# Performance work log

Hardware: AMD Instinct MI355X
Metric: run time of the kernel (lower is better)

The kernel has to match this reference:

```python
import jax, jax.numpy as jnp
import numpy as np

B, T, E, H = 8, 2048, 1024, 1024
_LN_EPS = 1e-3  # keras LayerNormalization default epsilon


def _ln(x, g, b):
    mu = jnp.mean(x, axis=-1, keepdims=True)
    var = jnp.var(x, axis=-1, keepdims=True)
    return (x - mu) * jax.lax.rsqrt(var + _LN_EPS) * g + b


def _time_shift(x):
    # ZeroPadding1D((1,0)) applied to x[:, :-1]: shift right by one, zero at t=0
    return jnp.pad(x[:, :-1], ((0, 0), (1, 0), (0, 0)))


def _wkv(k, v, w, u):
    """RWKV-v4 wkv: numerically stabilized exponential-decay recurrence.
    k, v: (B, T, H); w = -exp(time_decay) (negative), u = time_first: (H,).
    wkv_t = (sum_{i<t} e^{(t-1-i)w + k_i} v_i + e^{u + k_t} v_t)
          / (sum_{i<t} e^{(t-1-i)w + k_i}     + e^{u + k_t})
    """
    Bk, Tk, Hk = k.shape

    def step(carry, kv_t):
        aa, bb, pp = carry  # running num/den with shared log-scale pp
        kt, vt = kv_t
        ww = u + kt
        q = jnp.maximum(pp, ww)
        e1 = jnp.exp(pp - q)
        e2 = jnp.exp(ww - q)
        out = (e1 * aa + e2 * vt) / (e1 * bb + e2)
        ww2 = pp + w
        q2 = jnp.maximum(ww2, kt)
        e1b = jnp.exp(ww2 - q2)
        e2b = jnp.exp(kt - q2)
        return (e1b * aa + e2b * vt, e1b * bb + e2b, q2), out

    init = (jnp.zeros((Bk, Hk), k.dtype),
            jnp.zeros((Bk, Hk), k.dtype),
            jnp.full((Bk, Hk), -1e38, k.dtype))
    kT = jnp.swapaxes(k, 0, 1)  # (T, B, H)
    vT = jnp.swapaxes(v, 0, 1)
    _, outs = jax.lax.scan(step, init, (kT, vT))
    return jnp.swapaxes(outs, 0, 1)


def setup_inputs() -> dict:
    key = jax.random.key(0)
    ks = jax.random.split(key, 20)

    def glorot(k, shape):
        lim = np.sqrt(6.0 / (shape[0] + shape[1]))
        return jax.random.uniform(k, shape, jnp.float32, -lim, lim)

    return {
        'inputs': jax.random.normal(ks[0], (B, T, E), jnp.float32),
        'ln1_g': jnp.ones((E,), jnp.float32),
        'ln1_b': jnp.zeros((E,), jnp.float32),
        'ln2_g': jnp.ones((E,), jnp.float32),
        'ln2_b': jnp.zeros((E,), jnp.float32),
        'tm_mix_k': jax.random.uniform(ks[1], (E,), jnp.float32, 0.0, 2.0 / E),
        'tm_mix_v': jax.random.uniform(ks[2], (E,), jnp.float32, 0.0, 2.0 / E),
        'tm_mix_r': jax.random.uniform(ks[3], (E,), jnp.float32, 0.0, (2.0 / E) ** 0.5),
        'tm_Wk': glorot(ks[4], (E, H)),
        'tm_Wv': glorot(ks[5], (E, H)),
        'tm_Wr': glorot(ks[6], (E, H)),
        'time_decay': jax.random.uniform(ks[7], (H,), jnp.float32, 0.0, 0.5),
        'time_first': jax.random.uniform(ks[8], (H,), jnp.float32, 0.0, 0.05),
        'Wo': glorot(ks[9], (H, E)),
        'cm_mix_k': jax.random.uniform(ks[10], (E,), jnp.float32, 0.0, 2.0 / E),
        'cm_mix_r': jax.random.uniform(ks[11], (E,), jnp.float32, 0.0, 2.0 / E),
        'cm_Wk': glorot(ks[12], (E, 4 * H)),
        'cm_Wv': glorot(ks[13], (4 * H, E)),
        'cm_Wr': glorot(ks[14], (E, E)),
    }


def reference(inputs, ln1_g, ln1_b, ln2_g, ln2_b,
              tm_mix_k, tm_mix_v, tm_mix_r, tm_Wk, tm_Wv, tm_Wr,
              time_decay, time_first, Wo,
              cm_mix_k, cm_mix_r, cm_Wk, cm_Wv, cm_Wr):
    x = inputs

    # ---- time mixing ----
    h = _ln(x, ln1_g, ln1_b)
    h1 = _time_shift(h)
    xk = h * tm_mix_k + h1 * (1.0 - tm_mix_k)
    xv = h * tm_mix_v + h1 * (1.0 - tm_mix_v)
    xr = h * tm_mix_r + h1 * (1.0 - tm_mix_r)
    k = xk @ tm_Wk
    v = xv @ tm_Wv
    r = xr @ tm_Wr
    wkv = _wkv(k, v, -jnp.exp(time_decay), time_first)
    x = x + (jax.nn.sigmoid(r) * wkv) @ Wo

    # ---- channel mixing ----
    h = _ln(x, ln2_g, ln2_b)
    h1 = _time_shift(h)
    xk = h * cm_mix_k + h1 * (1.0 - cm_mix_k)
    xr = h * cm_mix_r + h1 * (1.0 - cm_mix_r)
    kc = jnp.square(jax.nn.relu(xk @ cm_Wk))  # (B, T, 4H)
    rc = jax.nn.sigmoid(xr @ cm_Wr)
    x = x + rc * (kc @ cm_Wv)
    return x
```

## Files before the change

### kernel.cpp

```cpp
#include <hip/hip_runtime.h>
#include <stdint.h>
#include <stddef.h>

#define Bb 8
#define Tt 2048
#define Ee 1024
#define Hh 1024
#define ROWS (Bb * Tt)
#define CC 32
#define LL 64

typedef __attribute__((ext_vector_type(8))) _Float16 half8v;
typedef __attribute__((ext_vector_type(4))) _Float16 half4v;
typedef __attribute__((ext_vector_type(4))) float f32x4;

#define GL2LDS(gp, lp)                                                        \
  __builtin_amdgcn_global_load_lds(                                          \
      (const __attribute__((address_space(1))) void*)(gp),                   \
      (__attribute__((address_space(3))) void*)(lp), 16, 0, 0)

#define VMCNT(n) __builtin_amdgcn_s_waitcnt(0xF70 | (n))

__global__ __launch_bounds__(256)
void wtrans_kernel(const float* __restrict__ W, _Float16* __restrict__ Wt,
                   const int K, const int N) {
  __shared__ float tle[64][65];
  const int ntn = N >> 6;
  const int tn = blockIdx.x % ntn;
  const int tk = blockIdx.x / ntn;
  const int tid = threadIdx.x;
  const int r = tid >> 4;
  const int c4 = (tid & 15) * 4;
#pragma unroll
  for (int i = 0; i < 4; i++) {
    const int row = r + i * 16;
    const float4 v = *reinterpret_cast<const float4*>(
        &W[(size_t)(tk * 64 + row) * N + tn * 64 + c4]);
    tle[row][c4] = v.x; tle[row][c4 + 1] = v.y;
    tle[row][c4 + 2] = v.z; tle[row][c4 + 3] = v.w;
  }
  __syncthreads();
#pragma unroll
  for (int j = 0; j < 2; j++) {
    const int ch = tid + j * 256;
    const int n = ch >> 3;
    const int k8 = (ch & 7) * 8;
    half8v o;
#pragma unroll
    for (int m = 0; m < 8; m++) o[m] = (_Float16)tle[k8 + m][n];
    *reinterpret_cast<half8v*>(&Wt[(size_t)(tn * 64 + n) * K + tk * 64 + k8]) = o;
  }
}

__global__ __launch_bounds__(256)
void ln_kernel(const float* __restrict__ x, const float* __restrict__ gw,
               const float* __restrict__ bw, _Float16* __restrict__ h) {
  const int row = blockIdx.x * 4 + (threadIdx.x >> 6);
  const int lane = threadIdx.x & 63;
  const float4* xr = reinterpret_cast<const float4*>(x + (size_t)row * Ee);
  float4 v[4];
  float s = 0.f, sq = 0.f;
#pragma unroll
  for (int i = 0; i < 4; i++) {
    v[i] = xr[lane + i * 64];
    s += v[i].x + v[i].y + v[i].z + v[i].w;
    sq += v[i].x * v[i].x + v[i].y * v[i].y + v[i].z * v[i].z + v[i].w * v[i].w;
  }
#pragma unroll
  for (int o = 32; o > 0; o >>= 1) {
    s += __shfl_xor(s, o);
    sq += __shfl_xor(sq, o);
  }
  const float mu = s * (1.f / Ee);
  const float var = sq * (1.f / Ee) - mu * mu;
  const float rs = rsqrtf(var + 1e-3f);
  const float4* gr = reinterpret_cast<const float4*>(gw);
  const float4* br = reinterpret_cast<const float4*>(bw);
#pragma unroll
  for (int i = 0; i < 4; i++) {
    const int c = lane + i * 64;
    const float4 g4 = gr[c], b4 = br[c];
    half4v o;
    o[0] = (_Float16)((v[i].x - mu) * rs * g4.x + b4.x);
    o[1] = (_Float16)((v[i].y - mu) * rs * g4.y + b4.y);
    o[2] = (_Float16)((v[i].z - mu) * rs * g4.z + b4.z);
    o[3] = (_Float16)((v[i].w - mu) * rs * g4.w + b4.w);
    *reinterpret_cast<half4v*>(&h[(size_t)row * Ee + (size_t)c * 4]) = o;
  }
}

template <bool HASV>
__global__ __launch_bounds__(256)
void mix_kernel(const _Float16* __restrict__ h, const float* __restrict__ mk,
                const float* __restrict__ mv, const float* __restrict__ mr,
                _Float16* __restrict__ xk, _Float16* __restrict__ xv,
                _Float16* __restrict__ xr) {
  const int gid = blockIdx.x * 256 + threadIdx.x;
  const int row = gid >> 8;
  const int c = gid & 255;
  const int t = row & (Tt - 1);
  const size_t o = (size_t)row * 1024 + (size_t)c * 4;
  const half4v hv4 = *reinterpret_cast<const half4v*>(&h[o]);
  float hx[4] = {(float)hv4[0], (float)hv4[1], (float)hv4[2], (float)hv4[3]};
  float h1[4] = {0.f, 0.f, 0.f, 0.f};
  if (t > 0) {
    const half4v p4 = *reinterpret_cast<const half4v*>(&h[o - 1024]);
    h1[0] = (float)p4[0]; h1[1] = (float)p4[1];
    h1[2] = (float)p4[2]; h1[3] = (float)p4[3];
  }
  const float4 k4 = reinterpret_cast<const float4*>(mk)[c];
  const float4 r4 = reinterpret_cast<const float4*>(mr)[c];
  const float km[4] = {k4.x, k4.y, k4.z, k4.w};
  const float rm[4] = {r4.x, r4.y, r4.z, r4.w};
  half4v ok, orr;
#pragma unroll
  for (int j = 0; j < 4; j++) {
    ok[j] = (_Float16)(hx[j] * km[j] + h1[j] * (1.f - km[j]));
    orr[j] = (_Float16)(hx[j] * rm[j] + h1[j] * (1.f - rm[j]));
  }
  *reinterpret_cast<half4v*>(&xk[o]) = ok;
  *reinterpret_cast<half4v*>(&xr[o]) = orr;
  if constexpr (HASV) {
    const float4 v4 = reinterpret_cast<const float4*>(mv)[c];
    const float vm[4] = {v4.x, v4.y, v4.z, v4.w};
    half4v ov;
#pragma unroll
    for (int j = 0; j < 4; j++)
      ov[j] = (_Float16)(hx[j] * vm[j] + h1[j] * (1.f - vm[j]));
    *reinterpret_cast<half4v*>(&xv[o]) = ov;
  }
}

__global__ __launch_bounds__(256)
void wkv_pass1(const _Float16* __restrict__ kb, const _Float16* __restrict__ vb,
               const float* __restrict__ decay,
               float* __restrict__ aal, float* __restrict__ bbl,
               float* __restrict__ ppl) {
  const int gid = blockIdx.x * 256 + threadIdx.x;
  const int h = gid & 1023;
  const int rest = gid >> 10;
  const int c = rest & (CC - 1);
  const int b = rest >> 5;
  const float w = -__expf(decay[h]);
  const size_t base = ((size_t)b * Tt + (size_t)c * LL) * Hh + h;
  float aa = 0.f, bb = 0.f, pp = -1e38f;
  for (int i0 = 0; i0 < LL; i0 += 8) {
    float kt[8], vt[8];
#pragma unroll
    for (int j = 0; j < 8; j++) {
      const size_t idx = base + (size_t)(i0 + j) * Hh;
      kt[j] = (float)kb[idx];
      vt[j] = (float)vb[idx];
    }
#pragma unroll
    for (int j = 0; j < 8; j++) {
      const float ww2 = pp + w;
      const float q2 = fmaxf(ww2, kt[j]);
      const float e1 = __expf(ww2 - q2);
      const float e2 = __expf(kt[j] - q2);
      aa = e1 * aa + e2 * vt[j];
      bb = e1 * bb + e2;
      pp = q2;
    }
  }
  const int sidx = (b * CC + c) * Hh + h;
  aal[sidx] = aa; bbl[sidx] = bb; ppl[sidx] = pp;
}

__global__ __launch_bounds__(256)
void wkv_pass2(const float* __restrict__ decay,
               const float* __restrict__ aal, const float* __restrict__ bbl,
               const float* __restrict__ ppl,
               float* __restrict__ aap, float* __restrict__ bbp,
               float* __restrict__ ppp) {
  const int gid = blockIdx.x * 256 + threadIdx.x;
  const int h = gid & 1023;
  const int b = gid >> 10;
  const float w = -__expf(decay[h]);
  const float Lw = (float)LL * w;
  float aa = 0.f, bb = 0.f, pp = -1e38f;
#pragma unroll
  for (int c = 0; c < CC; c++) {
    const int sidx = (b * CC + c) * Hh + h;
    aap[sidx] = aa; bbp[sidx] = bb; ppp[sidx] = pp;
    const float la = aal[sidx], lb = bbl[sidx], lp = ppl[sidx];
    const float sp = pp + Lw;
    const float q = fmaxf(sp, lp);
    const float e1 = __expf(sp - q);
    const float e2 = __expf(lp - q);
    aa = e1 * aa + e2 * la;
    bb = e1 * bb + e2 * lb;
    pp = q;
  }
}

__global__ __launch_bounds__(256)
void wkv_pass3(const _Float16* __restrict__ kb, const _Float16* __restrict__ vb,
               const _Float16* __restrict__ rb,
               const float* __restrict__ decay, const float* __restrict__ first,
               const float* __restrict__ aap, const float* __restrict__ bbp,
               const float* __restrict__ ppp, _Float16* __restrict__ ab) {
  const int gid = blockIdx.x * 256 + threadIdx.x;
  const int h = gid & 1023;
  const int rest = gid >> 10;
  const int c = rest & (CC - 1);
  const int b = rest >> 5;
  const float w = -__expf(decay[h]);
  const float u = first[h];
  const int sidx = (b * CC + c) * Hh + h;
  float aa = aap[sidx], bb = bbp[sidx], pp = ppp[sidx];
  const size_t base = ((size_t)b * Tt + (size_t)c * LL) * Hh + h;
  for (int i0 = 0; i0 < LL; i0 += 8) {
    float kt[8], vt[8], rr[8];
#pragma unroll
    for (int j = 0; j < 8; j++) {
      const size_t idx = base + (size_t)(i0 + j) * Hh;
      kt[j] = (float)kb[idx];
      vt[j] = (float)vb[idx];
      rr[j] = (float)rb[idx];
    }
#pragma unroll
    for (int j = 0; j < 8; j++) {
      const float ww = u + kt[j];
      const float q = fmaxf(pp, ww);
      const float e1 = __expf(pp - q);
      const float e2 = __expf(ww - q);
      const float out = (e1 * aa + e2 * vt[j]) / (e1 * bb + e2);
      const float sr = 1.f / (1.f + __expf(-rr[j]));
      ab[base + (size_t)(i0 + j) * Hh] = (_Float16)(sr * out);
      const float ww2 = pp + w;
      const float q2 = fmaxf(ww2, kt[j]);
      const float e1b = __expf(ww2 - q2);
      const float e2b = __expf(kt[j] - q2);
      aa = e1b * aa + e2b * vt[j];
      bb = e1b * bb + e2b;
      pp = q2;
    }
  }
}

template <int EPI>
__global__ __launch_bounds__(512, 2)
void gemm8(const _Float16* __restrict__ A, const int ldA,
           const _Float16* __restrict__ Bt, const int ldB,
           const int N, const int K, const int nbx,
           float* __restrict__ outF, _Float16* __restrict__ outH,
           const float* __restrict__ res, const _Float16* __restrict__ scale) {
  extern __shared__ _Float16 smem[];
  _Float16* sA = smem;
  _Float16* sB = smem + 2 * 16384;
  const int tid = threadIdx.x;
  const int lane = tid & 63;
  const int w = tid >> 6;
  const int wm = w >> 2, wn = w & 3;
  const int r0 = lane & 15, kg = lane >> 4;
  const int cpx = gridDim.x >> 3;
  const int wg = ((int)blockIdx.x & 7) * cpx + ((int)blockIdx.x >> 3);
  const int bm = (wg / nbx) * 256;
  const int bn = (wg % nbx) * 256;
  const int NT = K >> 6;

  f32x4 acc[8][4];
#pragma unroll
  for (int i = 0; i < 8; i++)
#pragma unroll
    for (int j = 0; j < 4; j++) acc[i][j] = (f32x4){0.f, 0.f, 0.f, 0.f};

  auto stage = [&](const _Float16* __restrict__ G, const int ldG,
                   const int growbase, const int t, _Float16* sX, const int hb) {
    _Float16* base = sX + (t & 1) * 16384 + hb * 8192;
#pragma unroll
    for (int i = 0; i < 2; i++) {
      const int rih = (w * 2 + i) * 8 + (lane >> 3);
      const int gs = (lane & 7) ^ (rih & 7);
      GL2LDS(G + (size_t)(growbase + hb * 128 + rih) * ldG + (size_t)t * 64 + gs * 8,
             base + (w * 2 + i) * 512);
    }
  };
  auto rdA = [&](int p, int row, int ks) -> half8v {
    return *reinterpret_cast<const half8v*>(
        sA + p * 16384 + row * 64 + ((ks ^ (row & 7)) << 3));
  };
  auto rdB = [&](int p, int row, int ks) -> half8v {
    return *reinterpret_cast<const half8v*>(
        sB + p * 16384 + row * 64 + ((ks ^ (row & 7)) << 3));
  };

  stage(A, ldA, bm, 0, sA, 0);
  stage(A, ldA, bm, 0, sA, 1);
  stage(Bt, ldB, bn, 0, sB, 1);
  stage(Bt, ldB, bn, 0, sB, 0);
  if (NT > 1) { stage(A, ldA, bm, 1, sA, 0); stage(A, ldA, bm, 1, sA, 1); }
  VMCNT(4);
  __builtin_amdgcn_s_barrier();
  __builtin_amdgcn_sched_barrier(0);

  for (int t = 0; t < NT; ++t) {
    const int p = t & 1;
    half8v a0[4][2], a1[4][2], b0[2][2], b1[2][2];
#pragma unroll
    for (int fr = 0; fr < 4; fr++)
#pragma unroll
      for (int kk = 0; kk < 2; kk++)
        a0[fr][kk] = rdA(p, wm * 128 + fr * 16 + r0, kk * 4 + kg);
#pragma unroll
    for (int fc = 0; fc < 2; fc++)
#pragma unroll
      for (int kk = 0; kk < 2; kk++)
        b0[fc][kk] = rdB(p, wn * 64 + fc * 16 + r0, kk * 4 + kg);
    if (t + 1 < NT) stage(Bt, ldB, bn, t + 1, sB, 1);
    __builtin_amdgcn_s_barrier();
    __builtin_amdgcn_sched_barrier(0);
    __builtin_amdgcn_s_setprio(1);
#pragma unroll
    for (int fr = 0; fr < 4; fr++)
#pragma unroll
      for (int fc = 0; fc < 2; fc++)
#pragma unroll
        for (int kk = 0; kk < 2; kk++)
          acc[fr][fc] = __builtin_amdgcn_mfma_f32_16x16x32_f16(
              a0[fr][kk], b0[fc][kk], acc[fr][fc], 0, 0, 0);
    __builtin_amdgcn_s_setprio(0);
    __builtin_amdgcn_sched_barrier(0);
    __builtin_amdgcn_s_barrier();
#pragma unroll
    for (int fr = 0; fr < 4; fr++)
#pragma unroll
      for (int kk = 0; kk < 2; kk++)
        a1[fr][kk] = rdA(p, wm * 128 + 64 + fr * 16 + r0, kk * 4 + kg);
#pragma unroll
    for (int fc = 0; fc < 2; fc++)
#pragma unroll
      for (int kk = 0; kk < 2; kk++)
        b1[fc][kk] = rdB(p, wn * 64 + 32 + fc * 16 + r0, kk * 4 + kg);
    if (t + 1 < NT) stage(Bt, ldB, bn, t + 1, sB, 0);
    __builtin_amdgcn_s_barrier();
    __builtin_amdgcn_sched_barrier(0);
    __builtin_amdgcn_s_setprio(1);
#pragma unroll
    for (int fr = 0; fr < 4; fr++)
#pragma unroll
      for (int fc = 0; fc < 2; fc++)
#pragma unroll
        for (int kk = 0; kk < 2; kk++)
          acc[4 + fr][fc] = __builtin_amdgcn_mfma_f32_16x16x32_f16(
              a1[fr][kk], b0[fc][kk], acc[4 + fr][fc], 0, 0, 0);
    __builtin_amdgcn_s_setprio(0);
    __builtin_amdgcn_sched_barrier(0);
    __builtin_amdgcn_s_barrier();
    if (t + 2 < NT) stage(A, ldA, bm, t + 2, sA, 0);
    __builtin_amdgcn_s_barrier();
    __builtin_amdgcn_sched_barrier(0);
    __builtin_amdgcn_s_setprio(1);
#pragma unroll
    for (int fr = 0; fr < 4; fr++)
#pragma unroll
      for (int fc = 0; fc < 2; fc++)
#pragma unroll
        for (int kk = 0; kk < 2; kk++)
          acc[4 + fr][2 + fc] = __builtin_amdgcn_mfma_f32_16x16x32_f16(
              a1[fr][kk], b1[fc][kk], acc[4 + fr][2 + fc], 0, 0, 0);
    __builtin_amdgcn_s_setprio(0);
    __builtin_amdgcn_sched_barrier(0);
    __builtin_amdgcn_s_barrier();
    if (t + 2 < NT) {
      stage(A, ldA, bm, t + 2, sA, 1);
      VMCNT(4);
    } else {
      VMCNT(0);
    }
    __builtin_amdgcn_s_barrier();
    __builtin_amdgcn_sched_barrier(0);
    __builtin_amdgcn_s_setprio(1);
#pragma unroll
    for (int fr = 0; fr < 4; fr++)
#pragma unroll
      for (int fc = 0; fc < 2; fc++)
#pragma unroll
        for (int kk = 0; kk < 2; kk++)
          acc[fr][2 + fc] = __builtin_amdgcn_mfma_f32_16x16x32_f16(
              a0[fr][kk], b1[fc][kk], acc[fr][2 + fc], 0, 0, 0);
    __builtin_amdgcn_s_setprio(0);
    __builtin_amdgcn_sched_barrier(0);
    __builtin_amdgcn_s_barrier();
  }
  VMCNT(0);

#pragma unroll
  for (int fr = 0; fr < 8; fr++) {
#pragma unroll
    for (int fc = 0; fc < 4; fc++) {
#pragma unroll
      for (int i = 0; i < 4; i++) {
        const int row = bm + wm * 128 + fr * 16 + (lane >> 4) * 4 + i;
        const int col = bn + wn * 64 + fc * 16 + r0;
        const size_t idx = (size_t)row * N + col;
        const float val = acc[fr][fc][i];
        if constexpr (EPI == 0) {
          outH[idx] = (_Float16)val;
        } else if constexpr (EPI == 1) {
          const float tt = fmaxf(val, 0.f);
          outH[idx] = (_Float16)(tt * tt);
        } else if constexpr (EPI == 2) {
          outH[idx] = (_Float16)(1.f / (1.f + __expf(-val)));
        } else if constexpr (EPI == 3) {
          outF[idx] = res[idx] + val;
        } else {
          outF[idx] = outF[idx] + (float)scale[idx] * val;
        }
      }
    }
  }
}

extern "C" void kernel_launch(void* const* d_in, const int* in_sizes, int n_in,
                              void* d_out, int out_size, void* d_ws,
                              size_t ws_size, hipStream_t stream) {
  (void)in_sizes; (void)n_in; (void)out_size; (void)ws_size;
  const float* x_in      = (const float*)d_in[0];
  const float* ln1_g     = (const float*)d_in[1];
  const float* ln1_b     = (const float*)d_in[2];
  const float* ln2_g     = (const float*)d_in[3];
  const float* ln2_b     = (const float*)d_in[4];
  const float* tm_mix_k  = (const float*)d_in[5];
  const float* tm_mix_v  = (const float*)d_in[6];
  const float* tm_mix_r  = (const float*)d_in[7];
  const float* tm_Wk     = (const float*)d_in[8];
  const float* tm_Wv     = (const float*)d_in[9];
  const float* tm_Wr     = (const float*)d_in[10];
  const float* time_decay= (const float*)d_in[11];
  const float* time_first= (const float*)d_in[12];
  const float* Wo        = (const float*)d_in[13];
  const float* cm_mix_k  = (const float*)d_in[14];
  const float* cm_mix_r  = (const float*)d_in[15];
  const float* cm_Wk     = (const float*)d_in[16];
  const float* cm_Wv     = (const float*)d_in[17];
  const float* cm_Wr     = (const float*)d_in[18];
  float* out = (float*)d_out;
  char* ws = (char*)d_ws;
  const size_t MB = 1024ull * 1024ull;

  _Float16* WkT   = (_Float16*)(ws + 0 * MB);
  _Float16* WvT   = (_Float16*)(ws + 2 * MB);
  _Float16* WrT   = (_Float16*)(ws + 4 * MB);
  _Float16* WoT   = (_Float16*)(ws + 6 * MB);
  _Float16* cmWkT = (_Float16*)(ws + 8 * MB);
  _Float16* cmWvT = (_Float16*)(ws + 16 * MB);
  _Float16* cmWrT = (_Float16*)(ws + 24 * MB);
  float* aal = (float*)(ws + 0 * MB);
  float* bbl = (float*)(ws + 1 * MB);
  float* ppl = (float*)(ws + 2 * MB);
  float* aap = (float*)(ws + 3 * MB);
  float* bbp = (float*)(ws + 4 * MB);
  float* ppp = (float*)(ws + 5 * MB);
  _Float16* h16   = (_Float16*)(ws + 26 * MB);
  _Float16* xk    = (_Float16*)(ws + 58 * MB);
  _Float16* xv    = (_Float16*)(ws + 90 * MB);
  _Float16* xr    = (_Float16*)(ws + 122 * MB);
  _Float16* kb    = h16;
  _Float16* vb    = xk;
  _Float16* rb    = xv;
  _Float16* ab    = xr;
  _Float16* h2    = (_Float16*)(ws + 26 * MB);
  _Float16* xr2   = (_Float16*)(ws + 58 * MB);
  _Float16* xk2   = (_Float16*)(ws + 90 * MB);
  _Float16* rc    = (_Float16*)(ws + 122 * MB);
  _Float16* kc    = (_Float16*)(ws + 26 * MB);

  const int SMEM = 131072;
  static bool attr_done = false;
  if (!attr_done) {
    hipFuncSetAttribute((const void*)gemm8<0>, hipFuncAttributeMaxDynamicSharedMemorySize, SMEM);
    hipFuncSetAttribute((const void*)gemm8<1>, hipFuncAttributeMaxDynamicSharedMemorySize, SMEM);
    hipFuncSetAttribute((const void*)gemm8<2>, hipFuncAttributeMaxDynamicSharedMemorySize, SMEM);
    hipFuncSetAttribute((const void*)gemm8<3>, hipFuncAttributeMaxDynamicSharedMemorySize, SMEM);
    hipFuncSetAttribute((const void*)gemm8<4>, hipFuncAttributeMaxDynamicSharedMemorySize, SMEM);
    attr_done = true;
  }

  wtrans_kernel<<<dim3(256), 256, 0, stream>>>(tm_Wk, WkT, 1024, 1024);
  wtrans_kernel<<<dim3(256), 256, 0, stream>>>(tm_Wv, WvT, 1024, 1024);
  wtrans_kernel<<<dim3(256), 256, 0, stream>>>(tm_Wr, WrT, 1024, 1024);
  wtrans_kernel<<<dim3(256), 256, 0, stream>>>(Wo, WoT, 1024, 1024);
  wtrans_kernel<<<dim3(1024), 256, 0, stream>>>(cm_Wk, cmWkT, 1024, 4096);
  wtrans_kernel<<<dim3(1024), 256, 0, stream>>>(cm_Wv, cmWvT, 4096, 1024);
  wtrans_kernel<<<dim3(256), 256, 0, stream>>>(cm_Wr, cmWrT, 1024, 1024);

  ln_kernel<<<dim3(ROWS / 4), 256, 0, stream>>>(x_in, ln1_g, ln1_b, h16);
  mix_kernel<true><<<dim3(ROWS), 256, 0, stream>>>(h16, tm_mix_k, tm_mix_v,
                                                   tm_mix_r, xk, xv, xr);
  gemm8<0><<<dim3(64 * 4), 512, SMEM, stream>>>(xk, 1024, WkT, 1024, 1024, 1024,
                                                4, nullptr, kb, nullptr, nullptr);
  gemm8<0><<<dim3(64 * 4), 512, SMEM, stream>>>(xv, 1024, WvT, 1024, 1024, 1024,
                                                4, nullptr, vb, nullptr, nullptr);
  gemm8<0><<<dim3(64 * 4), 512, SMEM, stream>>>(xr, 1024, WrT, 1024, 1024, 1024,
                                                4, nullptr, rb, nullptr, nullptr);
  wkv_pass1<<<dim3(Bb * CC * Hh / 256), 256, 0, stream>>>(kb, vb, time_decay,
                                                          aal, bbl, ppl);
  wkv_pass2<<<dim3(Bb * Hh / 256), 256, 0, stream>>>(time_decay, aal, bbl, ppl,
                                                     aap, bbp, ppp);
  wkv_pass3<<<dim3(Bb * CC * Hh / 256), 256, 0, stream>>>(
      kb, vb, rb, time_decay, time_first, aap, bbp, ppp, ab);
  gemm8<3><<<dim3(64 * 4), 512, SMEM, stream>>>(ab, 1024, WoT, 1024, 1024, 1024,
                                                4, out, nullptr, x_in, nullptr);

  ln_kernel<<<dim3(ROWS / 4), 256, 0, stream>>>(out, ln2_g, ln2_b, h2);
  mix_kernel<false><<<dim3(ROWS), 256, 0, stream>>>(h2, cm_mix_k, nullptr,
                                                    cm_mix_r, xk2, nullptr, xr2);
  gemm8<2><<<dim3(64 * 4), 512, SMEM, stream>>>(xr2, 1024, cmWrT, 1024, 1024,
                                                1024, 4, nullptr, rc, nullptr,
                                                nullptr);
  for (int half = 0; half < 2; half++) {
    const _Float16* Bk = cmWkT + (size_t)half * 2048 * 1024;
    const _Float16* Bv = cmWvT + (size_t)half * 2048;
    gemm8<1><<<dim3(64 * 8), 512, SMEM, stream>>>(xk2, 1024, Bk, 1024, 2048,
                                                  1024, 8, nullptr, kc, nullptr,
                                                  nullptr);
    gemm8<4><<<dim3(64 * 4), 512, SMEM, stream>>>(kc, 2048, Bv, 4096, 1024,
                                                  2048, 4, out, nullptr, nullptr,
                                                  rc);
  }
}
```

Before: 725.1 us.

## Collapse GEMM main loop into two phases with fewer barriers

Reworks the MFMA GEMM inner loop from four barrier-separated compute phases into two. All A and B fragments for the current k-tile are read from LDS up front, both halves of the next B tile are staged at loop start, and both halves of the A tile two steps ahead are staged together mid-loop. The aim is to cut the number of workgroup barriers and scheduling fences per iteration and give longer uninterrupted MFMA runs. In exchange, LDS reads and global-to-LDS traffic are issued in larger bursts, which may overlap less evenly with compute. Staging B earlier also depends on the double-buffer parity to avoid overwriting data still being read.

```diff
diff --git a/kernel.cpp b/kernel.cpp
--- a/kernel.cpp
+++ b/kernel.cpp
@@ -20,6 +20,8 @@
       (__attribute__((address_space(3))) void*)(lp), 16, 0, 0)
 
 #define VMCNT(n) __builtin_amdgcn_s_waitcnt(0xF70 | (n))
+#define BAR __builtin_amdgcn_s_barrier()
+#define SCHED0 __builtin_amdgcn_sched_barrier(0)
 
 __global__ __launch_bounds__(256)
 void wtrans_kernel(const float* __restrict__ W, _Float16* __restrict__ Wt,
@@ -292,25 +294,37 @@
   stage(Bt, ldB, bn, 0, sB, 0);
   if (NT > 1) { stage(A, ldA, bm, 1, sA, 0); stage(A, ldA, bm, 1, sA, 1); }
   VMCNT(4);
-  __builtin_amdgcn_s_barrier();
-  __builtin_amdgcn_sched_barrier(0);
+  BAR;
+  SCHED0;
 
   for (int t = 0; t < NT; ++t) {
     const int p = t & 1;
     half8v a0[4][2], a1[4][2], b0[2][2], b1[2][2];
+    if (t + 1 < NT) {
+      stage(Bt, ldB, bn, t + 1, sB, 1);
+      stage(Bt, ldB, bn, t + 1, sB, 0);
+    }
 #pragma unroll
     for (int fr = 0; fr < 4; fr++)
 #pragma unroll
       for (int kk = 0; kk < 2; kk++)
         a0[fr][kk] = rdA(p, wm * 128 + fr * 16 + r0, kk * 4 + kg);
 #pragma unroll
+    for (int fr = 0; fr < 4; fr++)
+#pragma unroll
+      for (int kk = 0; kk < 2; kk++)
+        a1[fr][kk] = rdA(p, wm * 128 + 64 + fr * 16 + r0, kk * 4 + kg);
+#pragma unroll
     for (int fc = 0; fc < 2; fc++)
 #pragma unroll
       for (int kk = 0; kk < 2; kk++)
         b0[fc][kk] = rdB(p, wn * 64 + fc * 16 + r0, kk * 4 + kg);
-    if (t + 1 < NT) stage(Bt, ldB, bn, t + 1, sB, 1);
-    __builtin_amdgcn_s_barrier();
-    __builtin_amdgcn_sched_barrier(0);
+#pragma unroll
+    for (int fc = 0; fc < 2; fc++)
+#pragma unroll
+      for (int kk = 0; kk < 2; kk++)
+        b1[fc][kk] = rdB(p, wn * 64 + 32 + fc * 16 + r0, kk * 4 + kg);
+    BAR;
     __builtin_amdgcn_s_setprio(1);
 #pragma unroll
     for (int fr = 0; fr < 4; fr++)
@@ -320,23 +334,6 @@
         for (int kk = 0; kk < 2; kk++)
           acc[fr][fc] = __builtin_amdgcn_mfma_f32_16x16x32_f16(
               a0[fr][kk], b0[fc][kk], acc[fr][fc], 0, 0, 0);
-    __builtin_amdgcn_s_setprio(0);
-    __builtin_amdgcn_sched_barrier(0);
-    __builtin_amdgcn_s_barrier();
-#pragma unroll
-    for (int fr = 0; fr < 4; fr++)
-#pragma unroll
-      for (int kk = 0; kk < 2; kk++)
-        a1[fr][kk] = rdA(p, wm * 128 + 64 + fr * 16 + r0, kk * 4 + kg);
-#pragma unroll
-    for (int fc = 0; fc < 2; fc++)
-#pragma unroll
-      for (int kk = 0; kk < 2; kk++)
-        b1[fc][kk] = rdB(p, wn * 64 + 32 + fc * 16 + r0, kk * 4 + kg);
-    if (t + 1 < NT) stage(Bt, ldB, bn, t + 1, sB, 0);
-    __builtin_amdgcn_s_barrier();
-    __builtin_amdgcn_sched_barrier(0);
-    __builtin_amdgcn_s_setprio(1);
 #pragma unroll
     for (int fr = 0; fr < 4; fr++)
 #pragma unroll
@@ -346,32 +343,25 @@
           acc[4 + fr][fc] = __builtin_amdgcn_mfma_f32_16x16x32_f16(
               a1[fr][kk], b0[fc][kk], acc[4 + fr][fc], 0, 0, 0);
     __builtin_amdgcn_s_setprio(0);
-    __builtin_amdgcn_sched_barrier(0);
-    __builtin_amdgcn_s_barrier();
-    if (t + 2 < NT) stage(A, ldA, bm, t + 2, sA, 0);
-    __builtin_amdgcn_s_barrier();
-    __builtin_amdgcn_sched_barrier(0);
-    __builtin_amdgcn_s_setprio(1);
-#pragma unroll
-    for (int fr = 0; fr < 4; fr++)
-#pragma unroll
-      for (int fc = 0; fc < 2; fc++)
-#pragma unroll
-        for (int kk = 0; kk < 2; kk++)
-          acc[4 + fr][2 + fc] = __builtin_amdgcn_mfma_f32_16x16x32_f16(
-              a1[fr][kk], b1[fc][kk], acc[4 + fr][2 + fc], 0, 0, 0);
-    __builtin_amdgcn_s_setprio(0);
-    __builtin_amdgcn_sched_barrier(0);
-    __builtin_amdgcn_s_barrier();
+    SCHED0;
+    BAR;
     if (t + 2 < NT) {
+      stage(A, ldA, bm, t + 2, sA, 0);
       stage(A, ldA, bm, t + 2, sA, 1);
       VMCNT(4);
     } else {
       VMCNT(0);
     }
-    __builtin_amdgcn_s_barrier();
-    __builtin_amdgcn_sched_barrier(0);
+    BAR;
     __builtin_amdgcn_s_setprio(1);
+#pragma unroll
+    for (int fr = 0; fr < 4; fr++)
+#pragma unroll
+      for (int fc = 0; fc < 2; fc++)
+#pragma unroll
+        for (int kk = 0; kk < 2; kk++)
+          acc[4 + fr][2 + fc] = __builtin_amdgcn_mfma_f32_16x16x32_f16(
+              a1[fr][kk], b1[fc][kk], acc[4 + fr][2 + fc], 0, 0, 0);
 #pragma unroll
     for (int fr = 0; fr < 4; fr++)
 #pragma unroll
@@ -381,8 +371,8 @@
           acc[fr][2 + fc] = __builtin_amdgcn_mfma_f32_16x16x32_f16(
               a0[fr][kk], b1[fc][kk], acc[fr][2 + fc], 0, 0, 0);
     __builtin_amdgcn_s_setprio(0);
-    __builtin_amdgcn_sched_barrier(0);
-    __builtin_amdgcn_s_barrier();
+    SCHED0;
+    BAR;
   }
   VMCNT(0);
 
```

Result: no change. 725.0 us (-0.0%).
